# Kernel tuning notes

Hardware: AMD Instinct MI355X
Metric: run time of the kernel (lower is better)

The kernel has to match this reference:

```python
import jax, jax.numpy as jnp
import numpy as np

SLOW = 32      # LSTM hidden size per weight-neuron
MSG = 16       # message size
MICRO = 2      # micro ticks per layer per step
LAYERS = [(256, 128), (128, 64)]
OUT_IDX = 0
EPS = 1e-6


def _lstm(x, h, c, Wi, Wh, b):
    g = x @ Wi + h @ Wh + b
    i, f, gg, o = jnp.split(g, 4, axis=-1)
    c = jax.nn.sigmoid(f) * c + jax.nn.sigmoid(i) * jnp.tanh(gg)
    h = jax.nn.sigmoid(o) * jnp.tanh(c)
    return h, c


def _ln(x, s, b):
    m = x.mean(-1, keepdims=True)
    v = ((x - m) ** 2).mean(-1, keepdims=True)
    return (x - m) * jax.lax.rsqrt(v + EPS) * s + b


def _merge(state):
    # mean-reduce first half of channels over batch, broadcast back
    half = state.shape[-1] // 2
    s1, s2 = state[..., :half], state[..., half:]
    s1 = jnp.broadcast_to(s1.mean(axis=0, keepdims=True), s1.shape)
    return jnp.concatenate([s1, s2], axis=-1)


def setup_inputs() -> dict:
    key = jax.random.key(0)
    ks = jax.random.split(key, 8)
    T, B = 4, 8
    sc = 0.1
    return {
        "inputs": jax.random.normal(ks[0], (T, B, LAYERS[0][0]), jnp.float32),
        "labels": jax.random.randint(ks[1], (T, B), 0, LAYERS[-1][1]),
        "Wi": jax.random.normal(ks[2], (2 * MSG, 4 * SLOW), jnp.float32) * sc,
        "Wh": jax.random.normal(ks[3], (SLOW, 4 * SLOW), jnp.float32) * sc,
        "b_lstm": jnp.zeros((4 * SLOW,), jnp.float32),
        "Wf": jax.random.normal(ks[4], (SLOW, MSG), jnp.float32) * sc,
        "bf": jnp.zeros((MSG,), jnp.float32),
        "Wb": jax.random.normal(ks[5], (SLOW, MSG), jnp.float32) * sc,
        "bwb": jnp.zeros((MSG,), jnp.float32),
        "ln_fs": jnp.ones((MSG,), jnp.float32),
        "ln_fb": jnp.zeros((MSG,), jnp.float32),
        "ln_bs": jnp.ones((MSG,), jnp.float32),
        "ln_bb": jnp.zeros((MSG,), jnp.float32),
    }


def reference(inputs, labels, Wi, Wh, b_lstm, Wf, bf, Wb, bwb,
              ln_fs, ln_fb, ln_bs, ln_bb):
    T, B, _ = inputs.shape
    n_out = LAYERS[-1][1]
    onehot = jax.nn.one_hot(labels, n_out, dtype=inputs.dtype)

    hs0 = tuple(jnp.zeros((B, i, o, SLOW), inputs.dtype) for i, o in LAYERS)
    cs0 = tuple(jnp.zeros((B, i, o, SLOW), inputs.dtype) for i, o in LAYERS)
    fwd0 = tuple(jnp.zeros((B, i, MSG), inputs.dtype) for i, o in LAYERS)
    bwd0 = tuple(jnp.zeros((B, o, MSG), inputs.dtype) for i, o in LAYERS)
    err0 = jnp.zeros((B, n_out, 2), inputs.dtype)

    def layer(h, c, f, bd):
        # h,c: (B,i,o,S); f: (B,i,M); bd: (B,o,M)
        Bq, ni, no, _ = h.shape
        x = jnp.concatenate([
            jnp.broadcast_to(f[:, :, None, :], (Bq, ni, no, MSG)),
            jnp.broadcast_to(bd[:, None, :, :], (Bq, ni, no, MSG)),
        ], axis=-1)  # (B,i,o,2M)
        for _ in range(MICRO):
            h, c = _lstm(x, h, c, Wi, Wh, b_lstm)
        fm = _ln(h @ Wf + bf, ln_fs, ln_fb)   # (B,i,o,M)
        bm = _ln(h @ Wb + bwb, ln_bs, ln_bb)  # (B,i,o,M)
        return h, c, fm.mean(axis=1), bm.mean(axis=2)

    def step(carry, x):
        hs, cs, fwd, bwd, error = carry
        inp, oh = x
        hs = [_merge(h) for h in hs]
        cs = [_merge(c) for c in cs]
        fwd = list(fwd)
        bwd = list(bwd)
        # inject input into channel 0 of first layer fwd msg
        fwd[0] = jnp.pad(inp[..., None], ((0, 0), (0, 0), (0, MSG - 1)))
        # inject 2-channel error into last layer bwd msg
        bwd[-1] = jnp.pad(error, ((0, 0), (0, 0), (0, MSG - 2)))
        out = None
        for i in range(len(LAYERS)):
            h, c, nf, nb = layer(hs[i], cs[i], fwd[i], bwd[i])
            hs[i], cs[i] = h, c
            if i > 0:
                bwd[i - 1] = nb.reshape(bwd[i - 1].shape)
            if i < len(LAYERS) - 1:
                fwd[i + 1] = nf.reshape(fwd[i + 1].shape)
            else:
                out = nf[..., OUT_IDX]  # (B, n_out)
        grad = jax.nn.softmax(out, axis=-1) - oh  # cross-entropy grad
        new_error = jnp.stack([grad, oh], axis=-1)  # feed_label=True
        return (tuple(hs), tuple(cs), tuple(fwd), tuple(bwd), new_error), out

    carry = (hs0, cs0, fwd0, bwd0, err0)
    _, outputs = jax.lax.scan(step, carry, (inputs, onehot))
    return outputs  # (T, B, n_out)
```

## Files before the change

kernel.cpp:

```cpp
#include <hip/hip_runtime.h>
#include <hip/hip_bf16.h>

#define SLOW 32
#define MSG 16
#define TSTEPS 4
#define BATCH 8
#define NI0 256
#define NO0 128
#define NI1 128
#define NO1 64

typedef __bf16 bf16x8 __attribute__((ext_vector_type(8)));
typedef float f32x4 __attribute__((ext_vector_type(4)));

__device__ __forceinline__ float rcpf(float x) { return __builtin_amdgcn_rcpf(x); }
__device__ __forceinline__ float sigf(float x) { return rcpf(1.f + __expf(-x)); }
__device__ __forceinline__ float tanh_apx(float x) {
    float xc = fminf(fmaxf(x, -15.f), 15.f);
    float e = __expf(-2.f * xc);
    return (1.f - e) * rcpf(1.f + e);
}
__device__ __forceinline__ unsigned short f2bf(float x) {
    __bf16 h = (__bf16)x;
    return __builtin_bit_cast(unsigned short, h);
}
__device__ __forceinline__ float bf2f(unsigned short u) {
    __bf16 h = __builtin_bit_cast(__bf16, u);
    return (float)h;
}
__device__ __forceinline__ float sum16(float v) {
    v += __shfl_xor(v, 1); v += __shfl_xor(v, 2);
    v += __shfl_xor(v, 4); v += __shfl_xor(v, 8);
    return v;
}

__global__ void k_prep(const float* __restrict__ Wh, const float* __restrict__ Wf,
                       const float* __restrict__ Wb, const float* __restrict__ Wi,
                       unsigned short* __restrict__ WhBp,
                       unsigned short* __restrict__ WfBp,
                       unsigned short* __restrict__ WbBp,
                       unsigned short* __restrict__ WiFp) {
    int i = blockIdx.x * 256 + threadIdx.x;
    if (i < 4096) {
        int e = i & 7, l = (i >> 3) & 63, nt = i >> 9;
        int k = (l >> 4) * 8 + e, col = nt * 16 + (l & 15);
        WhBp[i] = f2bf(Wh[k * 128 + col]);
    } else if (i < 4608) {
        int j = i - 4096;
        int e = j & 7, l = j >> 3;
        int k = (l >> 4) * 8 + e;
        WfBp[j] = f2bf(Wf[k * 16 + (l & 15)]);
    } else if (i < 5120) {
        int j = i - 4608;
        int e = j & 7, l = j >> 3;
        int k = (l >> 4) * 8 + e;
        WbBp[j] = f2bf(Wb[k * 16 + (l & 15)]);
    } else if (i < 9216) {
        int j = i - 5120;
        int e = j & 7, l = (j >> 3) & 63, nt = j >> 9;
        int k = (l >> 4) * 8 + e, col = nt * 16 + (l & 15);
        WiFp[j] = (k < 16) ? f2bf(Wi[k * 128 + col]) : (unsigned short)0;
    }
}

__global__ __launch_bounds__(256) void k_l0(
    const float* __restrict__ inp, const float* __restrict__ Wi,
    const unsigned short* __restrict__ WhBp, const float* __restrict__ b_lstm,
    const unsigned short* __restrict__ WfBp, const float* __restrict__ bf_,
    const float* __restrict__ ln_fs, const float* __restrict__ ln_fb,
    unsigned short* __restrict__ h0bf, float* __restrict__ c0g,
    const float* __restrict__ nb1, float* __restrict__ nf_part, int t) {
    int q = blockIdx.x & 1;
    int no = (blockIdx.x >> 1) & 127;
    int b = blockIdx.x >> 8;
    int tid = threadIdx.x;
    int w = __builtin_amdgcn_readfirstlane(tid >> 6);
    int l = tid & 63, lo = l & 15, hg = l >> 4;

    __shared__ unsigned short Hbf[128 * 40];
    __shared__ unsigned short BW[4096];
    __shared__ unsigned short BFr[512];
    __shared__ float gsh[128];
    __shared__ float mi_l[128];
    __shared__ float wi0[128];
    __shared__ float redn[4][16];

    {
        unsigned int* d = (unsigned int*)BW;
        const unsigned int* s = (const unsigned int*)WhBp;
#pragma unroll
        for (int i = tid; i < 2048; i += 256) d[i] = s[i];
        ((unsigned int*)BFr)[tid] = ((const unsigned int*)WfBp)[tid];
    }
    if (tid < 128) {
        float acc = b_lstm[tid];
        if (t > 0) {
            const float* nbr = nb1 + ((size_t)b * NO0 + no) * MSG;
#pragma unroll
            for (int m = 0; m < MSG; m++) acc += nbr[m] * Wi[(MSG + m) * 128 + tid];
        }
        gsh[tid] = acc;
        wi0[tid] = Wi[tid];
        mi_l[tid] = inp[((size_t)t * BATCH + b) * NI0 + q * 128 + tid];
    }
    {
        int lc = tid >> 1, half = tid & 1;
        unsigned int* hl = (unsigned int*)Hbf;
        if (t > 0) {
            const unsigned int* hsrc =
                (const unsigned int*)h0bf +
                ((size_t)(b * NO0 + no) * 256 + q * 128 + lc) * 16 + half * 8;
#pragma unroll
            for (int j = 0; j < 8; j++) hl[lc * 20 + half * 8 + j] = hsrc[j];
        } else {
#pragma unroll
            for (int j = 0; j < 8; j++) hl[lc * 20 + half * 8 + j] = 0u;
        }
    }
    size_t cbase = (size_t)(b * NO0 + no) * 256 * 32;
    float cst[2][4][2];
    if (t > 0) {
#pragma unroll
        for (int mi_ = 0; mi_ < 2; mi_++)
#pragma unroll
            for (int r = 0; r < 4; r++) {
                int gc = q * 128 + (w * 2 + mi_) * 16 + hg * 4 + r;
#pragma unroll
                for (int hi = 0; hi < 2; hi++)
                    cst[mi_][r][hi] = c0g[cbase + (size_t)gc * 32 + lo + 16 * hi];
            }
    } else {
#pragma unroll
        for (int mi_ = 0; mi_ < 2; mi_++)
#pragma unroll
            for (int r = 0; r < 4; r++) { cst[mi_][r][0] = 0.f; cst[mi_][r][1] = 0.f; }
    }
    __syncthreads();

    float g8[8], w8[8];
#pragma unroll
    for (int nt = 0; nt < 8; nt++) { g8[nt] = gsh[lo + 16 * nt]; w8[nt] = wi0[lo + 16 * nt]; }
    f32x4 miv[2];
#pragma unroll
    for (int mi_ = 0; mi_ < 2; mi_++)
#pragma unroll
        for (int r = 0; r < 4; r++)
            miv[mi_][r] = mi_l[(w * 2 + mi_) * 16 + hg * 4 + r];

#pragma unroll
    for (int micro = 0; micro < 2; micro++) {
#pragma unroll
        for (int mi_ = 0; mi_ < 2; mi_++) {
            int lt = w * 2 + mi_;
            bf16x8 A = *(const bf16x8*)&Hbf[(lt * 16 + lo) * 40 + hg * 8];
            f32x4 acc[4];
#pragma unroll
            for (int g = 0; g < 4; g++) {
                int nt = 2 * g;
                bf16x8 B = *(const bf16x8*)&BW[(nt * 64 + l) * 8];
                f32x4 ci = g8[nt] + miv[mi_] * w8[nt];
                acc[g] = __builtin_amdgcn_mfma_f32_16x16x32_bf16(A, B, ci, 0, 0, 0);
            }
#pragma unroll
            for (int r = 0; r < 4; r++) {
                int lrow = lt * 16 + hg * 4 + r;
                float cn = sigf(acc[1][r]) * cst[mi_][r][0] + sigf(acc[0][r]) * tanh_apx(acc[2][r]);
                cst[mi_][r][0] = cn;
                float hv = sigf(acc[3][r]) * tanh_apx(cn);
                Hbf[lrow * 40 + lo] = f2bf(hv);
                if (micro == 1)
                    c0g[cbase + (size_t)(q * 128 + lrow) * 32 + lo] = cn;
            }
#pragma unroll
            for (int g = 0; g < 4; g++) {
                int nt = 2 * g + 1;
                bf16x8 B = *(const bf16x8*)&BW[(nt * 64 + l) * 8];
                f32x4 ci = g8[nt] + miv[mi_] * w8[nt];
                acc[g] = __builtin_amdgcn_mfma_f32_16x16x32_bf16(A, B, ci, 0, 0, 0);
            }
#pragma unroll
            for (int r = 0; r < 4; r++) {
                int lrow = lt * 16 + hg * 4 + r;
                float cn = sigf(acc[1][r]) * cst[mi_][r][1] + sigf(acc[0][r]) * tanh_apx(acc[2][r]);
                cst[mi_][r][1] = cn;
                float hv = sigf(acc[3][r]) * tanh_apx(cn);
                Hbf[lrow * 40 + lo + 16] = f2bf(hv);
                if (micro == 1)
                    c0g[cbase + (size_t)(q * 128 + lrow) * 32 + lo + 16] = cn;
            }
        }
    }

    bf16x8 Ff = *(const bf16x8*)&BFr[l * 8];
    float lnfs = ln_fs[lo], lnfb = ln_fb[lo];
    float bfv = bf_[lo];
    f32x4 cif = {bfv, bfv, bfv, bfv};
    float nfp = 0.f;
#pragma unroll
    for (int mi_ = 0; mi_ < 2; mi_++) {
        int lt = w * 2 + mi_;
        bf16x8 A = *(const bf16x8*)&Hbf[(lt * 16 + lo) * 40 + hg * 8];
        f32x4 f = __builtin_amdgcn_mfma_f32_16x16x32_bf16(A, Ff, cif, 0, 0, 0);
#pragma unroll
        for (int r = 0; r < 4; r++) {
            float x = f[r];
            float mean = sum16(x) * 0.0625f;
            float d = x - mean;
            float rs = rsqrtf(sum16(d * d) * 0.0625f + 1e-6f);
            nfp += d * rs * lnfs + lnfb;
        }
    }
    nfp += __shfl_xor(nfp, 16);
    nfp += __shfl_xor(nfp, 32);
    if (l < 16) redn[w][l] = nfp;
    __syncthreads();
    if (tid < 16)
        nf_part[(((size_t)b * NO0 + no) * 2 + q) * 16 + tid] =
            redn[0][tid] + redn[1][tid] + redn[2][tid] + redn[3][tid];

    {
        int lc = tid >> 1, part = tid & 1;
        unsigned int* hdst =
            (unsigned int*)h0bf +
            ((size_t)(b * NO0 + no) * 256 + q * 128 + lc) * 16 + part * 8;
        const unsigned int* hl = (const unsigned int*)Hbf;
#pragma unroll
        for (int j = 0; j < 8; j++) hdst[j] = hl[lc * 20 + part * 8 + j];
    }
}

__global__ __launch_bounds__(256) void k_l1(
    const float* __restrict__ Wi, const unsigned short* __restrict__ WhBp,
    const float* __restrict__ b_lstm,
    const unsigned short* __restrict__ WfBp, const float* __restrict__ bf_,
    const float* __restrict__ ln_fs, const float* __restrict__ ln_fb,
    const unsigned short* __restrict__ WbBp, const float* __restrict__ bwb,
    const float* __restrict__ ln_bs, const float* __restrict__ ln_bb,
    const unsigned short* __restrict__ WiFp,
    unsigned short* __restrict__ h1bf, float* __restrict__ c1g,
    const float* __restrict__ nf_part, const float* __restrict__ gradP,
    const float* __restrict__ ohP,
    float* __restrict__ bm_g, float* __restrict__ outsum_part, int t) {
    int q = blockIdx.x & 1;
    int no = (blockIdx.x >> 1) & 63;
    int b = blockIdx.x >> 7;
    int tid = threadIdx.x;
    int w = __builtin_amdgcn_readfirstlane(tid >> 6);
    int l = tid & 63, lo = l & 15, hg = l >> 4;

    __shared__ unsigned short Hbf[64 * 40];
    __shared__ unsigned short BW[4096];
    __shared__ unsigned short WiF[4096];
    __shared__ unsigned short BFr[512];
    __shared__ unsigned short BBr[512];
    __shared__ float gsh[128];
    __shared__ float red[4];

    {
        unsigned int* d = (unsigned int*)BW;
        const unsigned int* s = (const unsigned int*)WhBp;
        unsigned int* d2 = (unsigned int*)WiF;
        const unsigned int* s2 = (const unsigned int*)WiFp;
#pragma unroll
        for (int i = tid; i < 2048; i += 256) { d[i] = s[i]; d2[i] = s2[i]; }
        ((unsigned int*)BFr)[tid] = ((const unsigned int*)WfBp)[tid];
        ((unsigned int*)BBr)[tid] = ((const unsigned int*)WbBp)[tid];
    }
    if (tid < 128) {
        float acc = b_lstm[tid];
        if (t > 0) {
            float g = gradP[b * NO1 + no], oh = ohP[b * NO1 + no];
            acc += g * Wi[MSG * 128 + tid] + oh * Wi[(MSG + 1) * 128 + tid];
        }
        gsh[tid] = acc;
    }
    {
        int lc = tid >> 2, part = tid & 3;
        unsigned int* hl = (unsigned int*)Hbf;
        if (t > 0) {
            const unsigned int* hsrc =
                (const unsigned int*)h1bf +
                ((size_t)(b * NO1 + no) * 128 + q * 64 + lc) * 16 + part * 4;
#pragma unroll
            for (int j = 0; j < 4; j++) hl[lc * 20 + part * 4 + j] = hsrc[j];
        } else {
#pragma unroll
            for (int j = 0; j < 4; j++) hl[lc * 20 + part * 4 + j] = 0u;
        }
    }
    size_t cbase = (size_t)(b * NO1 + no) * 128 * 32;
    float cst[4][2];
    if (t > 0) {
#pragma unroll
        for (int r = 0; r < 4; r++) {
            int gc = q * 64 + w * 16 + hg * 4 + r;
#pragma unroll
            for (int hi = 0; hi < 2; hi++)
                cst[r][hi] = c1g[cbase + (size_t)gc * 32 + lo + 16 * hi];
        }
    } else {
#pragma unroll
        for (int r = 0; r < 4; r++) { cst[r][0] = 0.f; cst[r][1] = 0.f; }
    }
    bf16x8 Anf;
#pragma unroll
    for (int e = 0; e < 8; e++) Anf[e] = (__bf16)0.f;
    if (hg < 2) {
        const float* p = nf_part +
            ((size_t)b * 128 + q * 64 + w * 16 + lo) * 32 + hg * 8;
#pragma unroll
        for (int e = 0; e < 8; e++)
            Anf[e] = (__bf16)((p[e] + p[e + 16]) * (1.f / 256.f));
    }
    __syncthreads();

    f32x4 xf4[8];
    {
        f32x4 zz = {0.f, 0.f, 0.f, 0.f};
#pragma unroll
        for (int nt = 0; nt < 8; nt++) {
            bf16x8 B = *(const bf16x8*)&WiF[(nt * 64 + l) * 8];
            xf4[nt] = __builtin_amdgcn_mfma_f32_16x16x32_bf16(Anf, B, zz, 0, 0, 0);
        }
    }
    float g8[8];
#pragma unroll
    for (int nt = 0; nt < 8; nt++) g8[nt] = gsh[lo + 16 * nt];

#pragma unroll
    for (int micro = 0; micro < 2; micro++) {
        bf16x8 A = *(const bf16x8*)&Hbf[(w * 16 + lo) * 40 + hg * 8];
        f32x4 acc[4];
#pragma unroll
        for (int g = 0; g < 4; g++) {
            int nt = 2 * g;
            bf16x8 B = *(const bf16x8*)&BW[(nt * 64 + l) * 8];
            f32x4 ci = xf4[nt] + g8[nt];
            acc[g] = __builtin_amdgcn_mfma_f32_16x16x32_bf16(A, B, ci, 0, 0, 0);
        }
#pragma unroll
        for (int r = 0; r < 4; r++) {
            float cn = sigf(acc[1][r]) * cst[r][0] + sigf(acc[0][r]) * tanh_apx(acc[2][r]);
            cst[r][0] = cn;
            float hv = sigf(acc[3][r]) * tanh_apx(cn);
            Hbf[(w * 16 + hg * 4 + r) * 40 + lo] = f2bf(hv);
            if (micro == 1)
                c1g[cbase + (size_t)(q * 64 + w * 16 + hg * 4 + r) * 32 + lo] = cn;
        }
#pragma unroll
        for (int g = 0; g < 4; g++) {
            int nt = 2 * g + 1;
            bf16x8 B = *(const bf16x8*)&BW[(nt * 64 + l) * 8];
            f32x4 ci = xf4[nt] + g8[nt];
            acc[g] = __builtin_amdgcn_mfma_f32_16x16x32_bf16(A, B, ci, 0, 0, 0);
        }
#pragma unroll
        for (int r = 0; r < 4; r++) {
            float cn = sigf(acc[1][r]) * cst[r][1] + sigf(acc[0][r]) * tanh_apx(acc[2][r]);
            cst[r][1] = cn;
            float hv = sigf(acc[3][r]) * tanh_apx(cn);
            Hbf[(w * 16 + hg * 4 + r) * 40 + lo + 16] = f2bf(hv);
            if (micro == 1)
                c1g[cbase + (size_t)(q * 64 + w * 16 + hg * 4 + r) * 32 + lo + 16] = cn;
        }
    }

    bf16x8 Ff = *(const bf16x8*)&BFr[l * 8];
    bf16x8 Bb = *(const bf16x8*)&BBr[l * 8];
    float lnfs = ln_fs[lo], lnfb = ln_fb[lo];
    float lnbs = ln_bs[lo], lnbb = ln_bb[lo];
    float bfv = bf_[lo], bwv = bwb[lo];
    f32x4 cif = {bfv, bfv, bfv, bfv};
    f32x4 cib = {bwv, bwv, bwv, bwv};
    float op = 0.f;
    {
        bf16x8 A = *(const bf16x8*)&Hbf[(w * 16 + lo) * 40 + hg * 8];
        f32x4 f = __builtin_amdgcn_mfma_f32_16x16x32_bf16(A, Ff, cif, 0, 0, 0);
        f32x4 g = __builtin_amdgcn_mfma_f32_16x16x32_bf16(A, Bb, cib, 0, 0, 0);
#pragma unroll
        for (int r = 0; r < 4; r++) {
            int gc = q * 64 + w * 16 + hg * 4 + r;
            {
                float x = f[r];
                float mean = sum16(x) * 0.0625f;
                float d = x - mean;
                float rs = rsqrtf(sum16(d * d) * 0.0625f + 1e-6f);
                op += d * rs * lnfs + lnfb;
            }
            {
                float x = g[r];
                float mean = sum16(x) * 0.0625f;
                float d = x - mean;
                float rs = rsqrtf(sum16(d * d) * 0.0625f + 1e-6f);
                bm_g[(((size_t)b * NO1 + no) * MSG + lo) * NI1 + gc] = d * rs * lnbs + lnbb;
            }
        }
    }
    op += __shfl_xor(op, 16);
    op += __shfl_xor(op, 32);
    if (l == 0) red[w] = op;
    __syncthreads();
    if (tid == 0)
        outsum_part[((size_t)b * NO1 + no) * 2 + q] = red[0] + red[1] + red[2] + red[3];

    {
        int lc = tid >> 2, part = tid & 3;
        unsigned int* hdst =
            (unsigned int*)h1bf +
            ((size_t)(b * NO1 + no) * 128 + q * 64 + lc) * 16 + part * 4;
        const unsigned int* hl = (const unsigned int*)Hbf;
#pragma unroll
        for (int j = 0; j < 4; j++) hdst[j] = hl[lc * 20 + part * 4 + j];
    }
}

__global__ __launch_bounds__(256) void k_step_end(
    unsigned int* __restrict__ h0, float* __restrict__ c0,
    unsigned int* __restrict__ h1, float* __restrict__ c1,
    const float* __restrict__ bm_g, float* __restrict__ nb1,
    const float* __restrict__ outsum_part, const int* __restrict__ labels,
    float* __restrict__ dout, float* __restrict__ gradP,
    float* __restrict__ ohP, int t) {
    int bid = blockIdx.x;
    if (bid < 1920) {
        int idx = bid * 256 + threadIdx.x;
        if (idx < 262144) {
            int u = idx & 7, cell = (idx >> 3) & 255, no = idx >> 11;
            size_t base = ((size_t)no * 256 + cell) * 16 + u;
            const size_t strd = (size_t)128 * 256 * 16;
            float s0 = 0.f, s1 = 0.f;
#pragma unroll
            for (int b = 0; b < 8; b++) {
                unsigned int v = h0[base + b * strd];
                s0 += bf2f((unsigned short)(v & 0xffff));
                s1 += bf2f((unsigned short)(v >> 16));
            }
            unsigned int mv = (unsigned int)f2bf(s0 * 0.125f) |
                              ((unsigned int)f2bf(s1 * 0.125f) << 16);
#pragma unroll
            for (int b = 0; b < 8; b++) h0[base + b * strd] = mv;
            return;
        }
        idx -= 262144;
        if (idx < 131072) {
            int s4 = idx & 3, cell = (idx >> 2) & 255, no = idx >> 10;
            float4* C = (float4*)c0;
            size_t base = ((size_t)no * 256 + cell) * 8 + s4;
            const size_t strd = (size_t)128 * 256 * 8;
            float4 a = {0.f, 0.f, 0.f, 0.f};
#pragma unroll
            for (int b = 0; b < 8; b++) {
                float4 v = C[base + b * strd];
                a.x += v.x; a.y += v.y; a.z += v.z; a.w += v.w;
            }
            a.x *= 0.125f; a.y *= 0.125f; a.z *= 0.125f; a.w *= 0.125f;
#pragma unroll
            for (int b = 0; b < 8; b++) C[base + b * strd] = a;
            return;
        }
        idx -= 131072;
        if (idx < 65536) {
            int u = idx & 7, cell = (idx >> 3) & 127, no = idx >> 10;
            size_t base = ((size_t)no * 128 + cell) * 16 + u;
            const size_t strd = (size_t)64 * 128 * 16;
            float s0 = 0.f, s1 = 0.f;
#pragma unroll
            for (int b = 0; b < 8; b++) {
                unsigned int v = h1[base + b * strd];
                s0 += bf2f((unsigned short)(v & 0xffff));
                s1 += bf2f((unsigned short)(v >> 16));
            }
            unsigned int mv = (unsigned int)f2bf(s0 * 0.125f) |
                              ((unsigned int)f2bf(s1 * 0.125f) << 16);
#pragma unroll
            for (int b = 0; b < 8; b++) h1[base + b * strd] = mv;
            return;
        }
        idx -= 65536;
        {
            int s4 = idx & 3, cell = (idx >> 2) & 127, no = idx >> 9;
            float4* C = (float4*)c1;
            size_t base = ((size_t)no * 128 + cell) * 8 + s4;
            const size_t strd = (size_t)64 * 128 * 8;
            float4 a = {0.f, 0.f, 0.f, 0.f};
#pragma unroll
            for (int b = 0; b < 8; b++) {
                float4 v = C[base + b * strd];
                a.x += v.x; a.y += v.y; a.z += v.z; a.w += v.w;
            }
            a.x *= 0.125f; a.y *= 0.125f; a.z *= 0.125f; a.w *= 0.125f;
#pragma unroll
            for (int b = 0; b < 8; b++) C[base + b * strd] = a;
        }
        return;
    }
    if (bid < 1984) {
        int g = (bid - 1920) * 256 + threadIdx.x;
        int ni = g & 127;
        int m = (g >> 7) & 15;
        int b = g >> 11;
        float a = 0.f;
#pragma unroll 8
        for (int no = 0; no < NO1; no++)
            a += bm_g[(((size_t)b * NO1 + no) * MSG + m) * NI1 + ni];
        nb1[((size_t)b * NI1 + ni) * MSG + m] = a * (1.f / NO1);
        return;
    }
    {
        int b = bid - 1984;
        int no = threadIdx.x;
        if (no < 64) {
            float v = (outsum_part[((size_t)b * NO1 + no) * 2] +
                       outsum_part[((size_t)b * NO1 + no) * 2 + 1]) * (1.f / 128.f);
            float mx = v;
#pragma unroll
            for (int d = 1; d < 64; d <<= 1) mx = fmaxf(mx, __shfl_xor(mx, d));
            float e = __expf(v - mx);
            float sum = e;
#pragma unroll
            for (int d = 1; d < 64; d <<= 1) sum += __shfl_xor(sum, d);
            int lbl = labels[t * BATCH + b];
            float oh = (no == lbl) ? 1.f : 0.f;
            gradP[b * NO1 + no] = e / sum - oh;
            ohP[b * NO1 + no] = oh;
            dout[((size_t)t * BATCH + b) * NO1 + no] = v;
        }
    }
}


extern "C" void kernel_launch(void* const* d_in, const int* in_sizes, int n_in,
                              void* d_out, int out_size, void* d_ws, size_t ws_size,
                              hipStream_t stream) {
    const float* inp   = (const float*)d_in[0];
    const int*   labels= (const int*)d_in[1];
    const float* Wi    = (const float*)d_in[2];
    const float* Wh    = (const float*)d_in[3];
    const float* b_lstm= (const float*)d_in[4];
    const float* Wf    = (const float*)d_in[5];
    const float* bf_   = (const float*)d_in[6];
    const float* Wb    = (const float*)d_in[7];
    const float* bwb   = (const float*)d_in[8];
    const float* ln_fs = (const float*)d_in[9];
    const float* ln_fb = (const float*)d_in[10];
    const float* ln_bs = (const float*)d_in[11];
    const float* ln_bb = (const float*)d_in[12];
    float* out = (float*)d_out;

    const size_t SZ0 = (size_t)BATCH * NO0 * 256 * 32;
    const size_t SZ1 = (size_t)BATCH * NO1 * 128 * 32;

    float* c0 = (float*)d_ws;
    float* c1 = c0 + SZ0;
    unsigned short* h0bf = (unsigned short*)(c1 + SZ1);
    unsigned short* h1bf = h0bf + SZ0;
    float* bm_g        = (float*)(h1bf + SZ1);
    float* nf_part     = bm_g + 1048576;
    float* nb1         = nf_part + 32768;
    float* outsum_part = nb1 + 16384;
    float* gradP       = outsum_part + 1024;
    float* ohP         = gradP + 512;
    unsigned short* WhBp = (unsigned short*)(ohP + 512);
    unsigned short* WfBp = WhBp + 4096;
    unsigned short* WbBp = WfBp + 512;
    unsigned short* WiFp = WbBp + 512;

    k_prep<<<36, 256, 0, stream>>>(Wh, Wf, Wb, Wi, WhBp, WfBp, WbBp, WiFp);

    for (int t = 0; t < TSTEPS; t++) {
        k_l0<<<BATCH * NO0 * 2, 256, 0, stream>>>(inp, Wi, WhBp, b_lstm, WfBp, bf_,
                                                  ln_fs, ln_fb, h0bf, c0, nb1,
                                                  nf_part, t);
        k_l1<<<BATCH * NO1 * 2, 256, 0, stream>>>(Wi, WhBp, b_lstm, WfBp, bf_,
                                                  ln_fs, ln_fb, WbBp, bwb, ln_bs, ln_bb,
                                                  WiFp, h1bf, c1, nf_part, gradP, ohP,
                                                  bm_g, outsum_part, t);
        k_step_end<<<1992, 256, 0, stream>>>((unsigned int*)h0bf, c0,
                                             (unsigned int*)h1bf, c1,
                                             bm_g, nb1, outsum_part, labels,
                                             out, gradP, ohP, t);
    }
}
```

Measured before the change: 296.0 us.

## Split LSTM layer kernels into single-wave blocks with register-held weights

```diff
diff --git a/kernel.cpp b/kernel.cpp
--- a/kernel.cpp
+++ b/kernel.cpp
@@ -63,53 +63,57 @@
     }
 }
 
-__global__ __launch_bounds__(256) void k_l0(
+__global__ __launch_bounds__(64) void k_l0(
     const float* __restrict__ inp, const float* __restrict__ Wi,
     const unsigned short* __restrict__ WhBp, const float* __restrict__ b_lstm,
     const unsigned short* __restrict__ WfBp, const float* __restrict__ bf_,
     const float* __restrict__ ln_fs, const float* __restrict__ ln_fb,
     unsigned short* __restrict__ h0bf, float* __restrict__ c0g,
     const float* __restrict__ nb1, float* __restrict__ nf_part, int t) {
-    int q = blockIdx.x & 1;
-    int no = (blockIdx.x >> 1) & 127;
-    int b = blockIdx.x >> 8;
-    int tid = threadIdx.x;
-    int w = __builtin_amdgcn_readfirstlane(tid >> 6);
-    int l = tid & 63, lo = l & 15, hg = l >> 4;
-
-    __shared__ unsigned short Hbf[128 * 40];
-    __shared__ unsigned short BW[4096];
-    __shared__ unsigned short BFr[512];
+    int bid = blockIdx.x;
+    int w4 = bid & 3;
+    int q = (bid >> 2) & 1;
+    int no = (bid >> 3) & 127;
+    int b = bid >> 10;
+    int l = threadIdx.x, lo = l & 15, hg = l >> 4;
+
+    __shared__ unsigned short Hbf[32 * 40];
     __shared__ float gsh[128];
-    __shared__ float mi_l[128];
-    __shared__ float wi0[128];
-    __shared__ float redn[4][16];
-
-    {
-        unsigned int* d = (unsigned int*)BW;
-        const unsigned int* s = (const unsigned int*)WhBp;
-#pragma unroll
-        for (int i = tid; i < 2048; i += 256) d[i] = s[i];
-        ((unsigned int*)BFr)[tid] = ((const unsigned int*)WfBp)[tid];
-    }
-    if (tid < 128) {
-        float acc = b_lstm[tid];
+
+    bf16x8 BWr[8];
+#pragma unroll
+    for (int nt = 0; nt < 8; nt++)
+        BWr[nt] = *(const bf16x8*)&WhBp[(nt * 64 + l) * 8];
+
+#pragma unroll
+    for (int gi = 0; gi < 2; gi++) {
+        int g = l + 64 * gi;
+        float acc = b_lstm[g];
         if (t > 0) {
             const float* nbr = nb1 + ((size_t)b * NO0 + no) * MSG;
 #pragma unroll
-            for (int m = 0; m < MSG; m++) acc += nbr[m] * Wi[(MSG + m) * 128 + tid];
-        }
-        gsh[tid] = acc;
-        wi0[tid] = Wi[tid];
-        mi_l[tid] = inp[((size_t)t * BATCH + b) * NI0 + q * 128 + tid];
-    }
-    {
-        int lc = tid >> 1, half = tid & 1;
+            for (int m = 0; m < MSG; m++) acc += nbr[m] * Wi[(MSG + m) * 128 + g];
+        }
+        gsh[g] = acc;
+    }
+
+    int cell0 = q * 128 + w4 * 32;
+    float w8[8];
+#pragma unroll
+    for (int nt = 0; nt < 8; nt++) w8[nt] = Wi[lo + 16 * nt];
+    f32x4 miv[2];
+#pragma unroll
+    for (int lt = 0; lt < 2; lt++)
+#pragma unroll
+        for (int r = 0; r < 4; r++)
+            miv[lt][r] = inp[((size_t)t * BATCH + b) * NI0 + cell0 + lt * 16 + hg * 4 + r];
+
+    {
+        int lc = l >> 1, half = l & 1;
         unsigned int* hl = (unsigned int*)Hbf;
         if (t > 0) {
-            const unsigned int* hsrc =
-                (const unsigned int*)h0bf +
-                ((size_t)(b * NO0 + no) * 256 + q * 128 + lc) * 16 + half * 8;
+            const unsigned int* hsrc = (const unsigned int*)h0bf +
+                ((size_t)(b * NO0 + no) * 256 + cell0 + lc) * 16 + half * 8;
 #pragma unroll
             for (int j = 0; j < 8; j++) hl[lc * 20 + half * 8 + j] = hsrc[j];
         } else {
@@ -117,88 +121,76 @@
             for (int j = 0; j < 8; j++) hl[lc * 20 + half * 8 + j] = 0u;
         }
     }
+
     size_t cbase = (size_t)(b * NO0 + no) * 256 * 32;
     float cst[2][4][2];
     if (t > 0) {
 #pragma unroll
-        for (int mi_ = 0; mi_ < 2; mi_++)
+        for (int lt = 0; lt < 2; lt++)
 #pragma unroll
             for (int r = 0; r < 4; r++) {
-                int gc = q * 128 + (w * 2 + mi_) * 16 + hg * 4 + r;
+                int gc = cell0 + lt * 16 + hg * 4 + r;
 #pragma unroll
                 for (int hi = 0; hi < 2; hi++)
-                    cst[mi_][r][hi] = c0g[cbase + (size_t)gc * 32 + lo + 16 * hi];
+                    cst[lt][r][hi] = c0g[cbase + (size_t)gc * 32 + lo + 16 * hi];
             }
     } else {
 #pragma unroll
-        for (int mi_ = 0; mi_ < 2; mi_++)
-#pragma unroll
-            for (int r = 0; r < 4; r++) { cst[mi_][r][0] = 0.f; cst[mi_][r][1] = 0.f; }
-    }
-    __syncthreads();
-
-    float g8[8], w8[8];
-#pragma unroll
-    for (int nt = 0; nt < 8; nt++) { g8[nt] = gsh[lo + 16 * nt]; w8[nt] = wi0[lo + 16 * nt]; }
-    f32x4 miv[2];
-#pragma unroll
-    for (int mi_ = 0; mi_ < 2; mi_++)
-#pragma unroll
-        for (int r = 0; r < 4; r++)
-            miv[mi_][r] = mi_l[(w * 2 + mi_) * 16 + hg * 4 + r];
+        for (int lt = 0; lt < 2; lt++)
+#pragma unroll
+            for (int r = 0; r < 4; r++) { cst[lt][r][0] = 0.f; cst[lt][r][1] = 0.f; }
+    }
+
+    float g8[8];
+#pragma unroll
+    for (int nt = 0; nt < 8; nt++) g8[nt] = gsh[lo + 16 * nt];
 
 #pragma unroll
     for (int micro = 0; micro < 2; micro++) {
 #pragma unroll
-        for (int mi_ = 0; mi_ < 2; mi_++) {
-            int lt = w * 2 + mi_;
+        for (int lt = 0; lt < 2; lt++) {
             bf16x8 A = *(const bf16x8*)&Hbf[(lt * 16 + lo) * 40 + hg * 8];
             f32x4 acc[4];
 #pragma unroll
             for (int g = 0; g < 4; g++) {
-                int nt = 2 * g;
-                bf16x8 B = *(const bf16x8*)&BW[(nt * 64 + l) * 8];
-                f32x4 ci = g8[nt] + miv[mi_] * w8[nt];
-                acc[g] = __builtin_amdgcn_mfma_f32_16x16x32_bf16(A, B, ci, 0, 0, 0);
+                f32x4 ci = g8[2 * g] + miv[lt] * w8[2 * g];
+                acc[g] = __builtin_amdgcn_mfma_f32_16x16x32_bf16(A, BWr[2 * g], ci, 0, 0, 0);
             }
 #pragma unroll
             for (int r = 0; r < 4; r++) {
                 int lrow = lt * 16 + hg * 4 + r;
-                float cn = sigf(acc[1][r]) * cst[mi_][r][0] + sigf(acc[0][r]) * tanh_apx(acc[2][r]);
-                cst[mi_][r][0] = cn;
+                float cn = sigf(acc[1][r]) * cst[lt][r][0] + sigf(acc[0][r]) * tanh_apx(acc[2][r]);
+                cst[lt][r][0] = cn;
                 float hv = sigf(acc[3][r]) * tanh_apx(cn);
                 Hbf[lrow * 40 + lo] = f2bf(hv);
                 if (micro == 1)
-                    c0g[cbase + (size_t)(q * 128 + lrow) * 32 + lo] = cn;
+                    c0g[cbase + (size_t)(cell0 + lrow) * 32 + lo] = cn;
             }
 #pragma unroll
             for (int g = 0; g < 4; g++) {
-                int nt = 2 * g + 1;
-                bf16x8 B = *(const bf16x8*)&BW[(nt * 64 + l) * 8];
-                f32x4 ci = g8[nt] + miv[mi_] * w8[nt];
-                acc[g] = __builtin_amdgcn_mfma_f32_16x16x32_bf16(A, B, ci, 0, 0, 0);
+                f32x4 ci = g8[2 * g + 1] + miv[lt] * w8[2 * g + 1];
+                acc[g] = __builtin_amdgcn_mfma_f32_16x16x32_bf16(A, BWr[2 * g + 1], ci, 0, 0, 0);
             }
 #pragma unroll
             for (int r = 0; r < 4; r++) {
                 int lrow = lt * 16 + hg * 4 + r;
-                float cn = sigf(acc[1][r]) * cst[mi_][r][1] + sigf(acc[0][r]) * tanh_apx(acc[2][r]);
-                cst[mi_][r][1] = cn;
+                float cn = sigf(acc[1][r]) * cst[lt][r][1] + sigf(acc[0][r]) * tanh_apx(acc[2][r]);
+                cst[lt][r][1] = cn;
                 float hv = sigf(acc[3][r]) * tanh_apx(cn);
                 Hbf[lrow * 40 + lo + 16] = f2bf(hv);
                 if (micro == 1)
-                    c0g[cbase + (size_t)(q * 128 + lrow) * 32 + lo + 16] = cn;
-            }
-        }
-    }
-
-    bf16x8 Ff = *(const bf16x8*)&BFr[l * 8];
+                    c0g[cbase + (size_t)(cell0 + lrow) * 32 + lo + 16] = cn;
+            }
+        }
+    }
+
+    bf16x8 Ff = *(const bf16x8*)&WfBp[l * 8];
     float lnfs = ln_fs[lo], lnfb = ln_fb[lo];
     float bfv = bf_[lo];
     f32x4 cif = {bfv, bfv, bfv, bfv};
     float nfp = 0.f;
 #pragma unroll
-    for (int mi_ = 0; mi_ < 2; mi_++) {
-        int lt = w * 2 + mi_;
+    for (int lt = 0; lt < 2; lt++) {
         bf16x8 A = *(const bf16x8*)&Hbf[(lt * 16 + lo) * 40 + hg * 8];
         f32x4 f = __builtin_amdgcn_mfma_f32_16x16x32_bf16(A, Ff, cif, 0, 0, 0);
 #pragma unroll
@@ -212,24 +204,20 @@
     }
     nfp += __shfl_xor(nfp, 16);
     nfp += __shfl_xor(nfp, 32);
-    if (l < 16) redn[w][l] = nfp;
-    __syncthreads();
-    if (tid < 16)
-        nf_part[(((size_t)b * NO0 + no) * 2 + q) * 16 + tid] =
-            redn[0][tid] + redn[1][tid] + redn[2][tid] + redn[3][tid];
-
-    {
-        int lc = tid >> 1, part = tid & 1;
-        unsigned int* hdst =
-            (unsigned int*)h0bf +
-            ((size_t)(b * NO0 + no) * 256 + q * 128 + lc) * 16 + part * 8;
+    if (l < 16)
+        nf_part[(((size_t)b * NO0 + no) * 8 + (q * 4 + w4)) * 16 + l] = nfp;
+
+    {
+        int lc = l >> 1, part = l & 1;
+        unsigned int* hdst = (unsigned int*)h0bf +
+            ((size_t)(b * NO0 + no) * 256 + cell0 + lc) * 16 + part * 8;
         const unsigned int* hl = (const unsigned int*)Hbf;
 #pragma unroll
         for (int j = 0; j < 8; j++) hdst[j] = hl[lc * 20 + part * 8 + j];
     }
 }
 
-__global__ __launch_bounds__(256) void k_l1(
+__global__ __launch_bounds__(64) void k_l1(
     const float* __restrict__ Wi, const unsigned short* __restrict__ WhBp,
     const float* __restrict__ b_lstm,
     const unsigned short* __restrict__ WfBp, const float* __restrict__ bf_,
@@ -241,46 +229,37 @@
     const float* __restrict__ nf_part, const float* __restrict__ gradP,
     const float* __restrict__ ohP,
     float* __restrict__ bm_g, float* __restrict__ outsum_part, int t) {
-    int q = blockIdx.x & 1;
-    int no = (blockIdx.x >> 1) & 63;
-    int b = blockIdx.x >> 7;
-    int tid = threadIdx.x;
-    int w = __builtin_amdgcn_readfirstlane(tid >> 6);
-    int l = tid & 63, lo = l & 15, hg = l >> 4;
-
-    __shared__ unsigned short Hbf[64 * 40];
-    __shared__ unsigned short BW[4096];
-    __shared__ unsigned short WiF[4096];
-    __shared__ unsigned short BFr[512];
-    __shared__ unsigned short BBr[512];
+    int bid = blockIdx.x;
+    int mt = bid & 7;
+    int no = (bid >> 3) & 63;
+    int b = bid >> 9;
+    int l = threadIdx.x, lo = l & 15, hg = l >> 4;
+
+    __shared__ unsigned short Hbf[16 * 40];
     __shared__ float gsh[128];
-    __shared__ float red[4];
-
-    {
-        unsigned int* d = (unsigned int*)BW;
-        const unsigned int* s = (const unsigned int*)WhBp;
-        unsigned int* d2 = (unsigned int*)WiF;
-        const unsigned int* s2 = (const unsigned int*)WiFp;
-#pragma unroll
-        for (int i = tid; i < 2048; i += 256) { d[i] = s[i]; d2[i] = s2[i]; }
-        ((unsigned int*)BFr)[tid] = ((const unsigned int*)WfBp)[tid];
-        ((unsigned int*)BBr)[tid] = ((const unsigned int*)WbBp)[tid];
-    }
-    if (tid < 128) {
-        float acc = b_lstm[tid];
+
+    bf16x8 BWr[8];
+#pragma unroll
+    for (int nt = 0; nt < 8; nt++)
+        BWr[nt] = *(const bf16x8*)&WhBp[(nt * 64 + l) * 8];
+
+#pragma unroll
+    for (int gi = 0; gi < 2; gi++) {
+        int g = l + 64 * gi;
+        float acc = b_lstm[g];
         if (t > 0) {
-            float g = gradP[b * NO1 + no], oh = ohP[b * NO1 + no];
-            acc += g * Wi[MSG * 128 + tid] + oh * Wi[(MSG + 1) * 128 + tid];
-        }
-        gsh[tid] = acc;
-    }
-    {
-        int lc = tid >> 2, part = tid & 3;
+            float gr = gradP[b * NO1 + no], oh = ohP[b * NO1 + no];
+            acc += gr * Wi[MSG * 128 + g] + oh * Wi[(MSG + 1) * 128 + g];
+        }
+        gsh[g] = acc;
+    }
+
+    {
+        int lc = l >> 2, part = l & 3;
         unsigned int* hl = (unsigned int*)Hbf;
         if (t > 0) {
-            const unsigned int* hsrc =
-                (const unsigned int*)h1bf +
-                ((size_t)(b * NO1 + no) * 128 + q * 64 + lc) * 16 + part * 4;
+            const unsigned int* hsrc = (const unsigned int*)h1bf +
+                ((size_t)(b * NO1 + no) * 128 + mt * 16 + lc) * 16 + part * 4;
 #pragma unroll
             for (int j = 0; j < 4; j++) hl[lc * 20 + part * 4 + j] = hsrc[j];
         } else {
@@ -288,12 +267,13 @@
             for (int j = 0; j < 4; j++) hl[lc * 20 + part * 4 + j] = 0u;
         }
     }
+
     size_t cbase = (size_t)(b * NO1 + no) * 128 * 32;
     float cst[4][2];
     if (t > 0) {
 #pragma unroll
         for (int r = 0; r < 4; r++) {
-            int gc = q * 64 + w * 16 + hg * 4 + r;
+            int gc = mt * 16 + hg * 4 + r;
 #pragma unroll
             for (int hi = 0; hi < 2; hi++)
                 cst[r][hi] = c1g[cbase + (size_t)gc * 32 + lo + 16 * hi];
@@ -302,24 +282,32 @@
 #pragma unroll
         for (int r = 0; r < 4; r++) { cst[r][0] = 0.f; cst[r][1] = 0.f; }
     }
+
     bf16x8 Anf;
 #pragma unroll
     for (int e = 0; e < 8; e++) Anf[e] = (__bf16)0.f;
     if (hg < 2) {
-        const float* p = nf_part +
-            ((size_t)b * 128 + q * 64 + w * 16 + lo) * 32 + hg * 8;
-#pragma unroll
-        for (int e = 0; e < 8; e++)
-            Anf[e] = (__bf16)((p[e] + p[e + 16]) * (1.f / 256.f));
-    }
-    __syncthreads();
+        const float* p = nf_part + ((size_t)b * NO0 + mt * 16 + lo) * 128;
+        float s[8];
+#pragma unroll
+        for (int e = 0; e < 8; e++) s[e] = 0.f;
+#pragma unroll
+        for (int j = 0; j < 8; j++) {
+            float4 a0 = *(const float4*)&p[j * 16 + hg * 8];
+            float4 a1 = *(const float4*)&p[j * 16 + hg * 8 + 4];
+            s[0] += a0.x; s[1] += a0.y; s[2] += a0.z; s[3] += a0.w;
+            s[4] += a1.x; s[5] += a1.y; s[6] += a1.z; s[7] += a1.w;
+        }
+#pragma unroll
+        for (int e = 0; e < 8; e++) Anf[e] = (__bf16)(s[e] * (1.f / 256.f));
+    }
 
     f32x4 xf4[8];
     {
         f32x4 zz = {0.f, 0.f, 0.f, 0.f};
 #pragma unroll
         for (int nt = 0; nt < 8; nt++) {
-            bf16x8 B = *(const bf16x8*)&WiF[(nt * 64 + l) * 8];
+            bf16x8 B = *(const bf16x8*)&WiFp[(nt * 64 + l) * 8];
             xf4[nt] = __builtin_amdgcn_mfma_f32_16x16x32_bf16(Anf, B, zz, 0, 0, 0);
         }
     }
@@ -329,44 +317,42 @@
 
 #pragma unroll
     for (int micro = 0; micro < 2; micro++) {
-        bf16x8 A = *(const bf16x8*)&Hbf[(w * 16 + lo) * 40 + hg * 8];
+        bf16x8 A = *(const bf16x8*)&Hbf[lo * 40 + hg * 8];
         f32x4 acc[4];
 #pragma unroll
         for (int g = 0; g < 4; g++) {
-            int nt = 2 * g;
-            bf16x8 B = *(const bf16x8*)&BW[(nt * 64 + l) * 8];
-            f32x4 ci = xf4[nt] + g8[nt];
-            acc[g] = __builtin_amdgcn_mfma_f32_16x16x32_bf16(A, B, ci, 0, 0, 0);
+            f32x4 ci = xf4[2 * g] + g8[2 * g];
+            acc[g] = __builtin_amdgcn_mfma_f32_16x16x32_bf16(A, BWr[2 * g], ci, 0, 0, 0);
         }
 #pragma unroll
         for (int r = 0; r < 4; r++) {
+            int gc = mt * 16 + hg * 4 + r;
             float cn = sigf(acc[1][r]) * cst[r][0] + sigf(acc[0][r]) * tanh_apx(acc[2][r]);
             cst[r][0] = cn;
             float hv = sigf(acc[3][r]) * tanh_apx(cn);
-            Hbf[(w * 16 + hg * 4 + r) * 40 + lo] = f2bf(hv);
+            Hbf[(hg * 4 + r) * 40 + lo] = f2bf(hv);
             if (micro == 1)
-                c1g[cbase + (size_t)(q * 64 + w * 16 + hg * 4 + r) * 32 + lo] = cn;
+                c1g[cbase + (size_t)gc * 32 + lo] = cn;
         }
 #pragma unroll
         for (int g = 0; g < 4; g++) {
-            int nt = 2 * g + 1;
-            bf16x8 B = *(const bf16x8*)&BW[(nt * 64 + l) * 8];
-            f32x4 ci = xf4[nt] + g8[nt];
-            acc[g] = __builtin_amdgcn_mfma_f32_16x16x32_bf16(A, B, ci, 0, 0, 0);
+            f32x4 ci = xf4[2 * g + 1] + g8[2 * g + 1];
+            acc[g] = __builtin_amdgcn_mfma_f32_16x16x32_bf16(A, BWr[2 * g + 1], ci, 0, 0, 0);
         }
 #pragma unroll
         for (int r = 0; r < 4; r++) {
+            int gc = mt * 16 + hg * 4 + r;
             float cn = sigf(acc[1][r]) * cst[r][1] + sigf(acc[0][r]) * tanh_apx(acc[2][r]);
             cst[r][1] = cn;
             float hv = sigf(acc[3][r]) * tanh_apx(cn);
-            Hbf[(w * 16 + hg * 4 + r) * 40 + lo + 16] = f2bf(hv);
+            Hbf[(hg * 4 + r) * 40 + lo + 16] = f2bf(hv);
             if (micro == 1)
-                c1g[cbase + (size_t)(q * 64 + w * 16 + hg * 4 + r) * 32 + lo + 16] = cn;
-        }
-    }
-
-    bf16x8 Ff = *(const bf16x8*)&BFr[l * 8];
-    bf16x8 Bb = *(const bf16x8*)&BBr[l * 8];
+                c1g[cbase + (size_t)gc * 32 + lo + 16] = cn;
+        }
+    }
+
+    bf16x8 Ff = *(const bf16x8*)&WfBp[l * 8];
+    bf16x8 Bb = *(const bf16x8*)&WbBp[l * 8];
     float lnfs = ln_fs[lo], lnfb = ln_fb[lo];
     float lnbs = ln_bs[lo], lnbb = ln_bb[lo];
     float bfv = bf_[lo], bwv = bwb[lo];
@@ -374,12 +360,12 @@
     f32x4 cib = {bwv, bwv, bwv, bwv};
     float op = 0.f;
     {
-        bf16x8 A = *(const bf16x8*)&Hbf[(w * 16 + lo) * 40 + hg * 8];
+        bf16x8 A = *(const bf16x8*)&Hbf[lo * 40 + hg * 8];
         f32x4 f = __builtin_amdgcn_mfma_f32_16x16x32_bf16(A, Ff, cif, 0, 0, 0);
         f32x4 g = __builtin_amdgcn_mfma_f32_16x16x32_bf16(A, Bb, cib, 0, 0, 0);
 #pragma unroll
         for (int r = 0; r < 4; r++) {
-            int gc = q * 64 + w * 16 + hg * 4 + r;
+            int gc = mt * 16 + hg * 4 + r;
             {
                 float x = f[r];
                 float mean = sum16(x) * 0.0625f;
@@ -398,16 +384,13 @@
     }
     op += __shfl_xor(op, 16);
     op += __shfl_xor(op, 32);
-    if (l == 0) red[w] = op;
-    __syncthreads();
-    if (tid == 0)
-        outsum_part[((size_t)b * NO1 + no) * 2 + q] = red[0] + red[1] + red[2] + red[3];
-
-    {
-        int lc = tid >> 2, part = tid & 3;
-        unsigned int* hdst =
-            (unsigned int*)h1bf +
-            ((size_t)(b * NO1 + no) * 128 + q * 64 + lc) * 16 + part * 4;
+    if (l == 0)
+        outsum_part[((size_t)b * NO1 + no) * 8 + mt] = op;
+
+    {
+        int lc = l >> 2, part = l & 3;
+        unsigned int* hdst = (unsigned int*)h1bf +
+            ((size_t)(b * NO1 + no) * 128 + mt * 16 + lc) * 16 + part * 4;
         const unsigned int* hl = (const unsigned int*)Hbf;
 #pragma unroll
         for (int j = 0; j < 4; j++) hdst[j] = hl[lc * 20 + part * 4 + j];
@@ -510,8 +493,11 @@
         int b = bid - 1984;
         int no = threadIdx.x;
         if (no < 64) {
-            float v = (outsum_part[((size_t)b * NO1 + no) * 2] +
-                       outsum_part[((size_t)b * NO1 + no) * 2 + 1]) * (1.f / 128.f);
+            const float* p = outsum_part + ((size_t)b * NO1 + no) * 8;
+            float v = 0.f;
+#pragma unroll
+            for (int j = 0; j < 8; j++) v += p[j];
+            v *= (1.f / 128.f);
             float mx = v;
 #pragma unroll
             for (int d = 1; d < 64; d <<= 1) mx = fmaxf(mx, __shfl_xor(mx, d));
@@ -556,9 +542,9 @@
     unsigned short* h1bf = h0bf + SZ0;
     float* bm_g        = (float*)(h1bf + SZ1);
     float* nf_part     = bm_g + 1048576;
-    float* nb1         = nf_part + 32768;
+    float* nb1         = nf_part + 131072;
     float* outsum_part = nb1 + 16384;
-    float* gradP       = outsum_part + 1024;
+    float* gradP       = outsum_part + 4096;
     float* ohP         = gradP + 512;
     unsigned short* WhBp = (unsigned short*)(ohP + 512);
     unsigned short* WfBp = WhBp + 4096;
@@ -568,13 +554,13 @@
     k_prep<<<36, 256, 0, stream>>>(Wh, Wf, Wb, Wi, WhBp, WfBp, WbBp, WiFp);
 
     for (int t = 0; t < TSTEPS; t++) {
-        k_l0<<<BATCH * NO0 * 2, 256, 0, stream>>>(inp, Wi, WhBp, b_lstm, WfBp, bf_,
-                                                  ln_fs, ln_fb, h0bf, c0, nb1,
-                                                  nf_part, t);
-        k_l1<<<BATCH * NO1 * 2, 256, 0, stream>>>(Wi, WhBp, b_lstm, WfBp, bf_,
-                                                  ln_fs, ln_fb, WbBp, bwb, ln_bs, ln_bb,
-                                                  WiFp, h1bf, c1, nf_part, gradP, ohP,
-                                                  bm_g, outsum_part, t);
+        k_l0<<<BATCH * NO0 * 2 * 4, 64, 0, stream>>>(inp, Wi, WhBp, b_lstm, WfBp, bf_,
+                                                     ln_fs, ln_fb, h0bf, c0, nb1,
+                                                     nf_part, t);
+        k_l1<<<BATCH * NO1 * 8, 64, 0, stream>>>(Wi, WhBp, b_lstm, WfBp, bf_,
+                                                 ln_fs, ln_fb, WbBp, bwb, ln_bs, ln_bb,
+                                                 WiFp, h1bf, c1, nf_part, gradP, ohP,
+                                                 bm_g, outsum_part, t);
         k_step_end<<<1992, 256, 0, stream>>>((unsigned int*)h0bf, c0,
                                              (unsigned int*)h1bf, c1,
                                              bm_g, nb1, outsum_part, labels,
```

Measured after the change: 305.8 us. 3.3% more time.
